# Kernel optimization log

Measured on AMD Instinct MI355X. Metric: run time of the kernel, lower is better.

## Reference

```python
import jax, jax.numpy as jnp
import numpy as np

B, C, H, W = 8, 96, 56, 56
N = H * W
K = 9
EPS = 1e-5

def _inorm(x):
    # InstanceNorm2d(affine=False): normalize over spatial dims per (batch, channel)
    m = jnp.mean(x, axis=(2, 3), keepdims=True)
    v = jnp.var(x, axis=(2, 3), keepdims=True)
    return (x - m) * jax.lax.rsqrt(v + EPS)

def _conv1(x, w, b):
    # 1x1 conv: (B,Cin,H,W) x (Cout,Cin) -> (B,Cout,H,W)
    return jnp.einsum('bchw,oc->bohw', x, w) + b[None, :, None, None]

def _grapher(x, rp, fc1_w, fc1_b, mr_w, mr_b, fc2_w, fc2_b):
    shortcut = x
    x = _inorm(_conv1(x, fc1_w, fc1_b))
    b, c, h, w = x.shape
    n = h * w
    xf = x.reshape(b, c, n)  # (B,C,N)
    # dynamic kNN on l2-normalized, gradient-stopped features (torch.no_grad + detach)
    xn = jax.lax.stop_gradient(xf)
    xn = xn / jnp.maximum(jnp.linalg.norm(xn, axis=1, keepdims=True), 1e-12)
    xt = jnp.swapaxes(xn, 1, 2)  # (B,N,C)
    sq = jnp.sum(xt * xt, axis=-1, keepdims=True)  # (B,N,1)
    dist = sq - 2.0 * jnp.einsum('bnc,bmc->bnm', xt, xt) + jnp.swapaxes(sq, 1, 2)
    dist = dist + rp  # relative_pos bias added to distances
    _, nn_idx = jax.lax.top_k(-dist, K)  # (B,N,K)
    # max-relative graph conv: gather neighbors, max over (x_j - x_i)
    x_j = jnp.take_along_axis(xf[:, :, None, :], nn_idx[:, None, :, :], axis=3)  # (B,C,N,K)
    xm = jnp.max(x_j - xf[:, :, :, None], axis=-1)  # (B,C,N)
    # channel-interleaved concat: (B,C,2,N,1) -> (B,2C,N,1)
    y = jnp.stack([xf, xm], axis=2).reshape(b, 2 * c, n, 1)
    y = jax.nn.gelu(_inorm(_conv1(y, mr_w, mr_b)), approximate=False)
    y = y.reshape(b, 2 * c, h, w)
    y = _inorm(_conv1(y, fc2_w, fc2_b))
    return y + shortcut

def _ffn(x, w1, b1, w2, b2):
    shortcut = x
    x = jax.nn.gelu(_inorm(_conv1(x, w1, b1)), approximate=False)
    x = _inorm(_conv1(x, w2, b2))
    return x + shortcut

_PARAM_SHAPES = [
    ('g1_fc1_w', (C, C)), ('g1_fc1_b', (C,)), ('g1_mr_w', (2*C, 2*C)), ('g1_mr_b', (2*C,)),
    ('g1_fc2_w', (C, 2*C)), ('g1_fc2_b', (C,)),
    ('g2_fc1_w', (C, C)), ('g2_fc1_b', (C,)), ('g2_mr_w', (2*C, 2*C)), ('g2_mr_b', (2*C,)),
    ('g2_fc2_w', (C, 2*C)), ('g2_fc2_b', (C,)),
    ('f1_fc1_w', (4*C, C)), ('f1_fc1_b', (4*C,)), ('f1_fc2_w', (C, 4*C)), ('f1_fc2_b', (C,)),
    ('f2_fc1_w', (4*C, C)), ('f2_fc1_b', (4*C,)), ('f2_fc2_w', (C, 4*C)), ('f2_fc2_b', (C,)),
]

def setup_inputs():
    key = jax.random.key(0)
    ks = jax.random.split(key, 2 + len(_PARAM_SHAPES))
    inp = {
        'x': jax.random.normal(ks[0], (B, C, H, W), dtype=jnp.float32),
        'relative_pos': jax.random.normal(ks[1], (1, N, N), dtype=jnp.float32) * 0.1,
    }
    for i, (nm, shp) in enumerate(_PARAM_SHAPES):
        inp[nm] = jax.random.normal(ks[i + 2], shp, dtype=jnp.float32) * 0.02
    return inp

def reference(x, relative_pos,
              g1_fc1_w, g1_fc1_b, g1_mr_w, g1_mr_b, g1_fc2_w, g1_fc2_b,
              g2_fc1_w, g2_fc1_b, g2_mr_w, g2_mr_b, g2_fc2_w, g2_fc2_b,
              f1_fc1_w, f1_fc1_b, f1_fc2_w, f1_fc2_b,
              f2_fc1_w, f2_fc1_b, f2_fc2_w, f2_fc2_b):
    y = _grapher(x, relative_pos, g1_fc1_w, g1_fc1_b, g1_mr_w, g1_mr_b, g1_fc2_w, g1_fc2_b)
    y = _ffn(y, f1_fc1_w, f1_fc1_b, f1_fc2_w, f1_fc2_b)
    y = jax.nn.relu(_inorm(y))
    y = _grapher(y, relative_pos, g2_fc1_w, g2_fc1_b, g2_mr_w, g2_mr_b, g2_fc2_w, g2_fc2_b)
    y = _ffn(y, f2_fc1_w, f2_fc1_b, f2_fc2_w, f2_fc2_b)
    y = _inorm(y)
    return x + y
```

## Files before the change

kernel.cpp:

```cpp
#include <hip/hip_runtime.h>
#include <math.h>

#define NN 3136
#define CC 96
#define BB 8
#define KNB 9
#define PARTS 7
#define FLT_MAX_ 3.402823466e+38f
typedef unsigned long long u64;

__global__ __launch_bounds__(256) void conv1_kernel(
    const float* __restrict__ in, const float* __restrict__ w,
    const float* __restrict__ bias, float* __restrict__ out, int K, int O)
{
    __shared__ float sW[16][64];
    __shared__ float sX[16][64];
    const int b  = blockIdx.z;
    const int n0 = blockIdx.x * 64;
    const int o0 = blockIdx.y * 64;
    const int tid = threadIdx.x;
    const int tx = tid & 15, ty = tid >> 4;
    const float* inb = in + (size_t)b * K * NN;

    float acc[4][4] = {{0.f}};

    for (int kb = 0; kb < K; kb += 16) {
        __syncthreads();
        {
            int o  = tid >> 2;
            int k4 = (tid & 3) << 2;
            float4 wv = make_float4(0.f, 0.f, 0.f, 0.f);
            if (o0 + o < O)
                wv = *(const float4*)&w[(size_t)(o0 + o) * K + kb + k4];
            sW[k4 + 0][o] = wv.x; sW[k4 + 1][o] = wv.y;
            sW[k4 + 2][o] = wv.z; sW[k4 + 3][o] = wv.w;
        }
        #pragma unroll
        for (int i = 0; i < 4; i++) {
            int e = tid + i * 256;
            int kk = e >> 6, n2 = e & 63;
            sX[kk][n2] = inb[(size_t)(kb + kk) * NN + n0 + n2];
        }
        __syncthreads();
        #pragma unroll
        for (int kk = 0; kk < 16; kk++) {
            const float4 av = *(const float4*)&sW[kk][ty << 2];
            const float4 xv = *(const float4*)&sX[kk][tx << 2];
            float a_[4] = {av.x, av.y, av.z, av.w};
            float x_[4] = {xv.x, xv.y, xv.z, xv.w};
            #pragma unroll
            for (int i = 0; i < 4; i++)
                #pragma unroll
                for (int j = 0; j < 4; j++)
                    acc[i][j] = fmaf(a_[i], x_[j], acc[i][j]);
        }
    }
    #pragma unroll
    for (int i = 0; i < 4; i++) {
        int o = o0 + (ty << 2) + i;
        if (o < O) {
            float bo = bias[o];
            float4 v = make_float4(acc[i][0] + bo, acc[i][1] + bo,
                                   acc[i][2] + bo, acc[i][3] + bo);
            *(float4*)&out[((size_t)b * O + o) * NN + n0 + (tx << 2)] = v;
        }
    }
}

__global__ __launch_bounds__(256) void inorm_kernel(
    const float* __restrict__ in, float* __restrict__ out,
    const float* __restrict__ res, int act)
{
    const int row = blockIdx.x;
    const float* x = in + (size_t)row * NN;
    const int tid = threadIdx.x;

    float v[13];
    float s = 0.f;
    #pragma unroll
    for (int i = 0; i < 13; i++) {
        int idx = tid + i * 256;
        v[i] = (idx < NN) ? x[idx] : 0.f;
        s += v[i];
    }
    __shared__ float red[4];
    #pragma unroll
    for (int off = 32; off > 0; off >>= 1) s += __shfl_down(s, off);
    if ((tid & 63) == 0) red[tid >> 6] = s;
    __syncthreads();
    const float mean = (red[0] + red[1] + red[2] + red[3]) * (1.f / (float)NN);

    float s2 = 0.f;
    #pragma unroll
    for (int i = 0; i < 13; i++) {
        int idx = tid + i * 256;
        if (idx < NN) { float d = v[i] - mean; s2 = fmaf(d, d, s2); }
    }
    #pragma unroll
    for (int off = 32; off > 0; off >>= 1) s2 += __shfl_down(s2, off);
    __syncthreads();
    if ((tid & 63) == 0) red[tid >> 6] = s2;
    __syncthreads();
    const float var = (red[0] + red[1] + red[2] + red[3]) * (1.f / (float)NN);
    const float rs = rsqrtf(var + 1e-5f);

    float* o = out + (size_t)row * NN;
    const float* rr = res ? (res + (size_t)row * NN) : nullptr;
    #pragma unroll
    for (int i = 0; i < 13; i++) {
        int idx = tid + i * 256;
        if (idx < NN) {
            float y = (v[i] - mean) * rs;
            if (act == 1)      y = 0.5f * y * (1.f + erff(y * 0.70710678118654752f));
            else if (act == 2) y = fmaxf(y, 0.f);
            if (rr) y += rr[idx];
            o[idx] = y;
        }
    }
}

__global__ __launch_bounds__(256) void colnorm_kernel(
    const float* __restrict__ xf, float* __restrict__ xn,
    float* __restrict__ sqc)
{
    const int g = blockIdx.x * 256 + threadIdx.x;
    const int b = g / NN;
    const int n = g - b * NN;
    const float* p = xf + (size_t)b * CC * NN + n;
    float* q = xn + (size_t)b * CC * NN + n;

    float s = 0.f;
    for (int c = 0; c < CC; c++) { float t = p[(size_t)c * NN]; s = fmaf(t, t, s); }
    const float den = fmaxf(sqrtf(s), 1e-12f);

    float sq = 0.f;
    for (int c = 0; c < CC; c++) {
        float t = p[(size_t)c * NN] / den;
        q[(size_t)c * NN] = t;
        sq = fmaf(t, t, sq);
    }
    sqc[g] = sq;
}

__device__ __forceinline__ u64 dkey(float d, int m)
{
    unsigned int ub = __float_as_uint(d);
    ub ^= (unsigned int)(((int)ub) >> 31) | 0x80000000u;
    return ((u64)ub << 32) | (unsigned int)m;
}
__device__ __forceinline__ void ins9u(u64 (&kk)[9], u64 key)
{
    if (key < kk[8]) {
        kk[8] = key;
        #pragma unroll
        for (int j = 8; j > 0; --j) {
            if (kk[j] < kk[j - 1]) {
                u64 t = kk[j]; kk[j] = kk[j - 1]; kk[j - 1] = t;
            }
        }
    }
}

__global__ __launch_bounds__(256) void knn_fused_kernel(
    const float* __restrict__ xn, const float* __restrict__ sqc,
    const float* __restrict__ rp, u64* __restrict__ pko)
{
    __shared__ float shR[CC * 64];
    __shared__ float shC[CC * 64];
    const int b    = blockIdx.z;
    const int part = blockIdx.y;
    const int r0   = blockIdx.x * 64;
    const int tid  = threadIdx.x;
    const int tx = tid & 7;
    const int ty = tid >> 3;
    const float* xb  = xn  + (size_t)b * CC * NN;
    const float* sqb = sqc + (size_t)b * NN;

    #pragma unroll
    for (int i = 0; i < 6; i++) {
        int idx = tid + i * 256;
        int c = idx >> 4, r4 = (idx & 15) << 2;
        *(float4*)&shR[c * 64 + r4] = *(const float4*)&xb[(size_t)c * NN + r0 + r4];
    }

    u64 kk0[9], kk1[9];
    #pragma unroll
    for (int j = 0; j < 9; j++) { kk0[j] = kk1[j] = 0xFFFFFFFFFFFFFFFFull; }

    const int rA = r0 + ty * 2;

    for (int mt = 0; mt < PARTS; mt++) {
        const int m0 = (part * PARTS + mt) * 64;

        const float4 s0 = *(const float4*)&sqb[m0 + tx * 8];
        const float4 s1 = *(const float4*)&sqb[m0 + tx * 8 + 4];
        const float4 a0 = *(const float4*)&rp[(size_t)rA * NN + m0 + tx * 8];
        const float4 a1 = *(const float4*)&rp[(size_t)rA * NN + m0 + tx * 8 + 4];
        const float4 b0v = *(const float4*)&rp[(size_t)(rA + 1) * NN + m0 + tx * 8];
        const float4 b1v = *(const float4*)&rp[(size_t)(rA + 1) * NN + m0 + tx * 8 + 4];

        __syncthreads();
        #pragma unroll
        for (int i = 0; i < 6; i++) {
            int idx = tid + i * 256;
            int c = idx >> 4, m4 = (idx & 15) << 2;
            *(float4*)&shC[c * 64 + m4] =
                *(const float4*)&xb[(size_t)c * NN + m0 + m4];
        }
        __syncthreads();

        float acc0[8] = {0.f, 0.f, 0.f, 0.f, 0.f, 0.f, 0.f, 0.f};
        float acc1[8] = {0.f, 0.f, 0.f, 0.f, 0.f, 0.f, 0.f, 0.f};
        #pragma unroll 4
        for (int c = 0; c < CC; c++) {
            const float2 rv = *(const float2*)&shR[c * 64 + ty * 2];
            const float4 c0 = *(const float4*)&shC[c * 64 + tx * 8];
            const float4 c1 = *(const float4*)&shC[c * 64 + tx * 8 + 4];
            acc0[0] = fmaf(rv.x, c0.x, acc0[0]);
            acc0[1] = fmaf(rv.x, c0.y, acc0[1]);
            acc0[2] = fmaf(rv.x, c0.z, acc0[2]);
            acc0[3] = fmaf(rv.x, c0.w, acc0[3]);
            acc0[4] = fmaf(rv.x, c1.x, acc0[4]);
            acc0[5] = fmaf(rv.x, c1.y, acc0[5]);
            acc0[6] = fmaf(rv.x, c1.z, acc0[6]);
            acc0[7] = fmaf(rv.x, c1.w, acc0[7]);
            acc1[0] = fmaf(rv.y, c0.x, acc1[0]);
            acc1[1] = fmaf(rv.y, c0.y, acc1[1]);
            acc1[2] = fmaf(rv.y, c0.z, acc1[2]);
            acc1[3] = fmaf(rv.y, c0.w, acc1[3]);
            acc1[4] = fmaf(rv.y, c1.x, acc1[4]);
            acc1[5] = fmaf(rv.y, c1.y, acc1[5]);
            acc1[6] = fmaf(rv.y, c1.z, acc1[6]);
            acc1[7] = fmaf(rv.y, c1.w, acc1[7]);
        }

        const float sq_[8] = {s0.x, s0.y, s0.z, s0.w, s1.x, s1.y, s1.z, s1.w};
        const float rA_[8] = {a0.x, a0.y, a0.z, a0.w, a1.x, a1.y, a1.z, a1.w};
        const float rB_[8] = {b0v.x, b0v.y, b0v.z, b0v.w, b1v.x, b1v.y, b1v.z, b1v.w};
        #pragma unroll
        for (int j = 0; j < 8; j++) {
            const int m = m0 + tx * 8 + j;
            ins9u(kk0, dkey(fmaf(-2.f, acc0[j], sq_[j] + rA_[j]), m));
            ins9u(kk1, dkey(fmaf(-2.f, acc1[j], sq_[j] + rB_[j]), m));
        }
    }

    const size_t base0 = ((size_t)(b * NN + rA)     * PARTS + part) * KNB;
    const size_t base1 = ((size_t)(b * NN + rA + 1) * PARTS + part) * KNB;
    #pragma unroll
    for (int k = 0; k < 9; k++) {
        u64 w = kk0[0];
        #pragma unroll
        for (int off = 1; off < 8; off <<= 1) {
            unsigned int lo = __shfl_xor((unsigned int)w, off);
            unsigned int hi = __shfl_xor((unsigned int)(w >> 32), off);
            u64 o = ((u64)hi << 32) | lo;
            w = (o < w) ? o : w;
        }
        if (kk0[0] == w) {
            #pragma unroll
            for (int j = 0; j < 8; j++) kk0[j] = kk0[j + 1];
            kk0[8] = 0xFFFFFFFFFFFFFFFFull;
        }
        if (tx == 0) pko[base0 + k] = w;
    }
    #pragma unroll
    for (int k = 0; k < 9; k++) {
        u64 w = kk1[0];
        #pragma unroll
        for (int off = 1; off < 8; off <<= 1) {
            unsigned int lo = __shfl_xor((unsigned int)w, off);
            unsigned int hi = __shfl_xor((unsigned int)(w >> 32), off);
            u64 o = ((u64)hi << 32) | lo;
            w = (o < w) ? o : w;
        }
        if (kk1[0] == w) {
            #pragma unroll
            for (int j = 0; j < 8; j++) kk1[j] = kk1[j + 1];
            kk1[8] = 0xFFFFFFFFFFFFFFFFull;
        }
        if (tx == 0) pko[base1 + k] = w;
    }
}

__global__ __launch_bounds__(256) void knn_merge_kernel(
    const u64* __restrict__ pko, int* __restrict__ nn_idx)
{
    const int g = blockIdx.x * 256 + threadIdx.x;
    if (g >= BB * NN) return;
    u64 kk[9];
    #pragma unroll
    for (int j = 0; j < 9; j++) kk[j] = 0xFFFFFFFFFFFFFFFFull;
    const u64* v = pko + (size_t)g * PARTS * KNB;
    for (int p = 0; p < PARTS; p++)
        #pragma unroll
        for (int j = 0; j < 9; j++)
            ins9u(kk, v[p * KNB + j]);
    #pragma unroll
    for (int j = 0; j < 9; j++)
        nn_idx[(size_t)g * KNB + j] = (int)(kk[j] & 0xFFFFFFFFu);
}

__global__ __launch_bounds__(256) void gather_kernel(
    const float* __restrict__ xf, const int* __restrict__ nn_idx,
    float* __restrict__ y)
{
    const size_t g = (size_t)blockIdx.x * 256 + threadIdx.x;
    const int n  = (int)(g % NN);
    const int bc = (int)(g / NN);
    const int c  = bc % CC;
    const int b  = bc / CC;
    const float* row = xf + (size_t)(b * CC + c) * NN;
    const float xi = row[n];
    const int* id = nn_idx + ((size_t)b * NN + n) * KNB;
    float mx = -FLT_MAX_;
    #pragma unroll
    for (int k = 0; k < KNB; k++) mx = fmaxf(mx, row[id[k]] - xi);
    float* o = y + ((size_t)b * 2 * CC + 2 * c) * NN + n;
    o[0]  = xi;
    o[NN] = mx;
}

static void conv1(const float* in, const float* w, const float* b, float* out,
                  int K, int O, hipStream_t s)
{
    dim3 grid(NN / 64, (O + 63) / 64, BB);
    conv1_kernel<<<grid, 256, 0, s>>>(in, w, b, out, K, O);
}
static void inorm(const float* in, float* out, const float* res, int ch, int act,
                  hipStream_t s)
{
    inorm_kernel<<<BB * ch, 256, 0, s>>>(in, out, res, act);
}

struct GrapherP {
    const float *fc1w, *fc1b, *mrw, *mrb, *fc2w, *fc2b;
};

static void run_grapher(const float* in, const float* rp, const GrapherP& p,
                        float* outCur, float* bufA, float* bufB, float* xnb,
                        float* sqc, int* idx, hipStream_t s)
{
    conv1(in, p.fc1w, p.fc1b, bufA, CC, CC, s);
    inorm(bufA, bufB, nullptr, CC, 0, s);
    colnorm_kernel<<<(BB * NN) / 256, 256, 0, s>>>(bufB, xnb, sqc);
    u64* pko = (u64*)bufA;
    knn_fused_kernel<<<dim3(NN / 64, PARTS, BB), 256, 0, s>>>(xnb, sqc, rp, pko);
    knn_merge_kernel<<<(BB * NN + 255) / 256, 256, 0, s>>>(pko, idx);
    gather_kernel<<<(BB * CC * NN) / 256, 256, 0, s>>>(bufB, idx, bufA);
    conv1(bufA, p.mrw, p.mrb, bufB, 2 * CC, 2 * CC, s);
    inorm(bufB, bufA, nullptr, 2 * CC, 1, s);
    conv1(bufA, p.fc2w, p.fc2b, bufB, 2 * CC, CC, s);
    inorm(bufB, outCur, in, CC, 0, s);
}

static void run_ffn(const float* in, const float* w1, const float* b1,
                    const float* w2, const float* b2,
                    float* outCur, float* bufA, float* bufB, hipStream_t s)
{
    conv1(in, w1, b1, bufA, CC, 4 * CC, s);
    inorm(bufA, bufB, nullptr, 4 * CC, 1, s);
    conv1(bufB, w2, b2, bufA, 2 * CC * 2, CC, s);
    inorm(bufA, outCur, in, CC, 0, s);
}

extern "C" void kernel_launch(void* const* d_in, const int* in_sizes, int n_in,
                              void* d_out, int out_size, void* d_ws, size_t ws_size,
                              hipStream_t stream)
{
    const float* x  = (const float*)d_in[0];
    const float* rp = (const float*)d_in[1];
    GrapherP g1 = {(const float*)d_in[2],  (const float*)d_in[3],
                   (const float*)d_in[4],  (const float*)d_in[5],
                   (const float*)d_in[6],  (const float*)d_in[7]};
    GrapherP g2 = {(const float*)d_in[8],  (const float*)d_in[9],
                   (const float*)d_in[10], (const float*)d_in[11],
                   (const float*)d_in[12], (const float*)d_in[13]};
    const float* f1w1 = (const float*)d_in[14]; const float* f1b1 = (const float*)d_in[15];
    const float* f1w2 = (const float*)d_in[16]; const float* f1b2 = (const float*)d_in[17];
    const float* f2w1 = (const float*)d_in[18]; const float* f2b1 = (const float*)d_in[19];
    const float* f2w2 = (const float*)d_in[20]; const float* f2b2 = (const float*)d_in[21];
    float* out = (float*)d_out;

    const size_t P  = (size_t)BB * CC * NN;
    const size_t P4 = 4 * P;
    float* ws   = (float*)d_ws;
    float* bufA = ws;
    float* bufB = bufA + P4;
    float* xnb  = bufB + P4;
    float* cur0 = xnb + P;
    float* cur1 = cur0 + P;
    float* sqc  = cur1 + P;
    int*   idx  = (int*)(sqc + (size_t)BB * NN);

    run_grapher(x, rp, g1, cur0, bufA, bufB, xnb, sqc, idx, stream);
    run_ffn(cur0, f1w1, f1b1, f1w2, f1b2, cur1, bufA, bufB, stream);
    inorm(cur1, cur0, nullptr, CC, 2, stream);
    run_grapher(cur0, rp, g2, cur1, bufA, bufB, xnb, sqc, idx, stream);
    run_ffn(cur1, f2w1, f2b1, f2w2, f2b2, cur0, bufA, bufB, stream);
    inorm(cur0, out, x, CC, 0, stream);
    (void)in_sizes; (void)n_in; (void)out_size; (void)ws_size;
}
```

Baseline: 1.300 ms.

## Retile kNN distance kernel to 4x4 per thread and prefetch next column tile

Changes the kNN distance tile so each thread computes 4 rows by 4 columns instead of 2 by 8. Each thread now keeps four 9-entry top-k lists, and the final shuffle reduction runs across 16 lanes instead of 8. The next column tile of features is also prefetched into registers while the current tile is computed, to hide global load latency. This raises register pressure substantially (36 u64 top-k entries per thread), which may lower occupancy or cause spills, and it doubles the number of insertion lists each thread maintains.

```diff
diff --git a/kernel.cpp b/kernel.cpp
--- a/kernel.cpp
+++ b/kernel.cpp
@@ -171,8 +171,8 @@
     const int part = blockIdx.y;
     const int r0   = blockIdx.x * 64;
     const int tid  = threadIdx.x;
-    const int tx = tid & 7;
-    const int ty = tid >> 3;
+    const int tx = tid & 15;
+    const int ty = tid >> 4;
     const float* xb  = xn  + (size_t)b * CC * NN;
     const float* sqb = sqc + (size_t)b * NN;
 
@@ -183,103 +183,99 @@
         *(float4*)&shR[c * 64 + r4] = *(const float4*)&xb[(size_t)c * NN + r0 + r4];
     }
 
-    u64 kk0[9], kk1[9];
-    #pragma unroll
-    for (int j = 0; j < 9; j++) { kk0[j] = kk1[j] = 0xFFFFFFFFFFFFFFFFull; }
-
-    const int rA = r0 + ty * 2;
-
-    for (int mt = 0; mt < PARTS; mt++) {
-        const int m0 = (part * PARTS + mt) * 64;
-
-        const float4 s0 = *(const float4*)&sqb[m0 + tx * 8];
-        const float4 s1 = *(const float4*)&sqb[m0 + tx * 8 + 4];
-        const float4 a0 = *(const float4*)&rp[(size_t)rA * NN + m0 + tx * 8];
-        const float4 a1 = *(const float4*)&rp[(size_t)rA * NN + m0 + tx * 8 + 4];
-        const float4 b0v = *(const float4*)&rp[(size_t)(rA + 1) * NN + m0 + tx * 8];
-        const float4 b1v = *(const float4*)&rp[(size_t)(rA + 1) * NN + m0 + tx * 8 + 4];
-
-        __syncthreads();
+    u64 kk[4][9];
+    #pragma unroll
+    for (int i = 0; i < 4; i++)
+        #pragma unroll
+        for (int j = 0; j < 9; j++) kk[i][j] = 0xFFFFFFFFFFFFFFFFull;
+
+    const int rA = r0 + ty * 4;
+
+    float4 nx[6];
+    {
+        const int m0 = part * PARTS * 64;
         #pragma unroll
         for (int i = 0; i < 6; i++) {
             int idx = tid + i * 256;
             int c = idx >> 4, m4 = (idx & 15) << 2;
-            *(float4*)&shC[c * 64 + m4] =
-                *(const float4*)&xb[(size_t)c * NN + m0 + m4];
-        }
+            nx[i] = *(const float4*)&xb[(size_t)c * NN + m0 + m4];
+        }
+    }
+
+    for (int mt = 0; mt < PARTS; mt++) {
+        const int m0 = (part * PARTS + mt) * 64;
+
         __syncthreads();
-
-        float acc0[8] = {0.f, 0.f, 0.f, 0.f, 0.f, 0.f, 0.f, 0.f};
-        float acc1[8] = {0.f, 0.f, 0.f, 0.f, 0.f, 0.f, 0.f, 0.f};
+        #pragma unroll
+        for (int i = 0; i < 6; i++) {
+            int idx = tid + i * 256;
+            int c = idx >> 4, m4 = (idx & 15) << 2;
+            *(float4*)&shC[c * 64 + m4] = nx[i];
+        }
+        if (mt + 1 < PARTS) {
+            const int m0n = m0 + 64;
+            #pragma unroll
+            for (int i = 0; i < 6; i++) {
+                int idx = tid + i * 256;
+                int c = idx >> 4, m4 = (idx & 15) << 2;
+                nx[i] = *(const float4*)&xb[(size_t)c * NN + m0n + m4];
+            }
+        }
+        const float4 sqv = *(const float4*)&sqb[m0 + tx * 4];
+        const float4 rp0 = *(const float4*)&rp[(size_t)(rA + 0) * NN + m0 + tx * 4];
+        const float4 rp1 = *(const float4*)&rp[(size_t)(rA + 1) * NN + m0 + tx * 4];
+        const float4 rp2 = *(const float4*)&rp[(size_t)(rA + 2) * NN + m0 + tx * 4];
+        const float4 rp3 = *(const float4*)&rp[(size_t)(rA + 3) * NN + m0 + tx * 4];
+        __syncthreads();
+
+        float acc[4][4] = {{0.f}};
         #pragma unroll 4
         for (int c = 0; c < CC; c++) {
-            const float2 rv = *(const float2*)&shR[c * 64 + ty * 2];
-            const float4 c0 = *(const float4*)&shC[c * 64 + tx * 8];
-            const float4 c1 = *(const float4*)&shC[c * 64 + tx * 8 + 4];
-            acc0[0] = fmaf(rv.x, c0.x, acc0[0]);
-            acc0[1] = fmaf(rv.x, c0.y, acc0[1]);
-            acc0[2] = fmaf(rv.x, c0.z, acc0[2]);
-            acc0[3] = fmaf(rv.x, c0.w, acc0[3]);
-            acc0[4] = fmaf(rv.x, c1.x, acc0[4]);
-            acc0[5] = fmaf(rv.x, c1.y, acc0[5]);
-            acc0[6] = fmaf(rv.x, c1.z, acc0[6]);
-            acc0[7] = fmaf(rv.x, c1.w, acc0[7]);
-            acc1[0] = fmaf(rv.y, c0.x, acc1[0]);
-            acc1[1] = fmaf(rv.y, c0.y, acc1[1]);
-            acc1[2] = fmaf(rv.y, c0.z, acc1[2]);
-            acc1[3] = fmaf(rv.y, c0.w, acc1[3]);
-            acc1[4] = fmaf(rv.y, c1.x, acc1[4]);
-            acc1[5] = fmaf(rv.y, c1.y, acc1[5]);
-            acc1[6] = fmaf(rv.y, c1.z, acc1[6]);
-            acc1[7] = fmaf(rv.y, c1.w, acc1[7]);
-        }
-
-        const float sq_[8] = {s0.x, s0.y, s0.z, s0.w, s1.x, s1.y, s1.z, s1.w};
-        const float rA_[8] = {a0.x, a0.y, a0.z, a0.w, a1.x, a1.y, a1.z, a1.w};
-        const float rB_[8] = {b0v.x, b0v.y, b0v.z, b0v.w, b1v.x, b1v.y, b1v.z, b1v.w};
-        #pragma unroll
-        for (int j = 0; j < 8; j++) {
-            const int m = m0 + tx * 8 + j;
-            ins9u(kk0, dkey(fmaf(-2.f, acc0[j], sq_[j] + rA_[j]), m));
-            ins9u(kk1, dkey(fmaf(-2.f, acc1[j], sq_[j] + rB_[j]), m));
-        }
-    }
-
-    const size_t base0 = ((size_t)(b * NN + rA)     * PARTS + part) * KNB;
-    const size_t base1 = ((size_t)(b * NN + rA + 1) * PARTS + part) * KNB;
-    #pragma unroll
-    for (int k = 0; k < 9; k++) {
-        u64 w = kk0[0];
-        #pragma unroll
-        for (int off = 1; off < 8; off <<= 1) {
-            unsigned int lo = __shfl_xor((unsigned int)w, off);
-            unsigned int hi = __shfl_xor((unsigned int)(w >> 32), off);
-            u64 o = ((u64)hi << 32) | lo;
-            w = (o < w) ? o : w;
-        }
-        if (kk0[0] == w) {
-            #pragma unroll
-            for (int j = 0; j < 8; j++) kk0[j] = kk0[j + 1];
-            kk0[8] = 0xFFFFFFFFFFFFFFFFull;
-        }
-        if (tx == 0) pko[base0 + k] = w;
-    }
-    #pragma unroll
-    for (int k = 0; k < 9; k++) {
-        u64 w = kk1[0];
-        #pragma unroll
-        for (int off = 1; off < 8; off <<= 1) {
-            unsigned int lo = __shfl_xor((unsigned int)w, off);
-            unsigned int hi = __shfl_xor((unsigned int)(w >> 32), off);
-            u64 o = ((u64)hi << 32) | lo;
-            w = (o < w) ? o : w;
-        }
-        if (kk1[0] == w) {
-            #pragma unroll
-            for (int j = 0; j < 8; j++) kk1[j] = kk1[j + 1];
-            kk1[8] = 0xFFFFFFFFFFFFFFFFull;
-        }
-        if (tx == 0) pko[base1 + k] = w;
+            const float4 rv = *(const float4*)&shR[c * 64 + ty * 4];
+            const float4 cv = *(const float4*)&shC[c * 64 + tx * 4];
+            const float r_[4] = {rv.x, rv.y, rv.z, rv.w};
+            const float c_[4] = {cv.x, cv.y, cv.z, cv.w};
+            #pragma unroll
+            for (int i = 0; i < 4; i++)
+                #pragma unroll
+                for (int j = 0; j < 4; j++)
+                    acc[i][j] = fmaf(r_[i], c_[j], acc[i][j]);
+        }
+
+        const float sq_[4] = {sqv.x, sqv.y, sqv.z, sqv.w};
+        const float rpv[4][4] = {{rp0.x, rp0.y, rp0.z, rp0.w},
+                                 {rp1.x, rp1.y, rp1.z, rp1.w},
+                                 {rp2.x, rp2.y, rp2.z, rp2.w},
+                                 {rp3.x, rp3.y, rp3.z, rp3.w}};
+        #pragma unroll
+        for (int i = 0; i < 4; i++)
+            #pragma unroll
+            for (int j = 0; j < 4; j++) {
+                const int m = m0 + tx * 4 + j;
+                ins9u(kk[i], dkey(fmaf(-2.f, acc[i][j], sq_[j] + rpv[i][j]), m));
+            }
+    }
+
+    #pragma unroll
+    for (int i = 0; i < 4; i++) {
+        const size_t base = ((size_t)(b * NN + rA + i) * PARTS + part) * KNB;
+        #pragma unroll
+        for (int k = 0; k < 9; k++) {
+            u64 w = kk[i][0];
+            #pragma unroll
+            for (int off = 1; off < 16; off <<= 1) {
+                unsigned int lo = __shfl_xor((unsigned int)w, off);
+                unsigned int hi = __shfl_xor((unsigned int)(w >> 32), off);
+                u64 o = ((u64)hi << 32) | lo;
+                w = (o < w) ? o : w;
+            }
+            if (kk[i][0] == w) {
+                #pragma unroll
+                for (int j = 0; j < 8; j++) kk[i][j] = kk[i][j + 1];
+                kk[i][8] = 0xFFFFFFFFFFFFFFFFull;
+            }
+            if (tx == 0) pko[base + k] = w;
+        }
     }
 }
 
```

Measured after the change: 1.509 ms. 1.16x slower.

## Compute kNN distance Gram matrix with bf16x3 split MFMA instead of FP32 FMA

Applied to the files above, without the earlier changes.

Normalized features are split into three bf16 parts (high, mid, low) and stored row-major. The kNN kernel then computes the pairwise dot products with six 16x16x32 bf16 MFMA products per K chunk, which approximates FP32 accuracy, replacing the scalar FP32 FMA tile loop. The block grows to 512 threads, each handling one row and 4 columns per 32-column tile, with results staged through shared memory before top-9 insertion. The aim is to move the dominant N^2*C GEMM onto matrix cores. The cost is extra split/conversion work, more syncs per tile, and a small risk of precision-induced neighbor tie flips.

```diff
diff --git a/kernel.cpp b/kernel.cpp
--- a/kernel.cpp
+++ b/kernel.cpp
@@ -8,6 +8,9 @@
 #define PARTS 7
 #define FLT_MAX_ 3.402823466e+38f
 typedef unsigned long long u64;
+typedef unsigned short ushortT;
+typedef __attribute__((ext_vector_type(8))) short short8;
+typedef __attribute__((ext_vector_type(4))) float f32x4;
 
 __global__ __launch_bounds__(256) void conv1_kernel(
     const float* __restrict__ in, const float* __restrict__ w,
@@ -119,25 +122,41 @@
     }
 }
 
+__device__ __forceinline__ unsigned bf16rne(float x)
+{
+    unsigned u = __float_as_uint(x);
+    return (u + 0x7fffu + ((u >> 16) & 1u)) >> 16;
+}
+
 __global__ __launch_bounds__(256) void colnorm_kernel(
-    const float* __restrict__ xf, float* __restrict__ xn,
+    const float* __restrict__ xf, ushortT* __restrict__ xh,
+    ushortT* __restrict__ xm, ushortT* __restrict__ xl,
     float* __restrict__ sqc)
 {
     const int g = blockIdx.x * 256 + threadIdx.x;
     const int b = g / NN;
     const int n = g - b * NN;
     const float* p = xf + (size_t)b * CC * NN + n;
-    float* q = xn + (size_t)b * CC * NN + n;
 
     float s = 0.f;
     for (int c = 0; c < CC; c++) { float t = p[(size_t)c * NN]; s = fmaf(t, t, s); }
     const float den = fmaxf(sqrtf(s), 1e-12f);
 
+    const size_t o = (size_t)g * CC;
     float sq = 0.f;
     for (int c = 0; c < CC; c++) {
         float t = p[(size_t)c * NN] / den;
-        q[(size_t)c * NN] = t;
         sq = fmaf(t, t, sq);
+        unsigned hr = bf16rne(t);
+        float hf = __uint_as_float(hr << 16);
+        float r1 = t - hf;
+        unsigned mr = bf16rne(r1);
+        float mf = __uint_as_float(mr << 16);
+        float r2 = r1 - mf;
+        unsigned lr = bf16rne(r2);
+        xh[o + c] = (ushortT)hr;
+        xm[o + c] = (ushortT)mr;
+        xl[o + c] = (ushortT)lr;
     }
     sqc[g] = sq;
 }
@@ -161,125 +180,112 @@
     }
 }
 
-__global__ __launch_bounds__(256) void knn_fused_kernel(
-    const float* __restrict__ xn, const float* __restrict__ sqc,
+__global__ __launch_bounds__(512, 4) void knn_mfma_kernel(
+    const ushortT* __restrict__ xh, const ushortT* __restrict__ xm,
+    const ushortT* __restrict__ xl, const float* __restrict__ sqc,
     const float* __restrict__ rp, u64* __restrict__ pko)
 {
-    __shared__ float shR[CC * 64];
-    __shared__ float shC[CC * 64];
+    __shared__ ushortT shA[3][64][104];
+    __shared__ ushortT shB[3][32][104];
+    __shared__ float   shD[64][33];
     const int b    = blockIdx.z;
     const int part = blockIdx.y;
     const int r0   = blockIdx.x * 64;
     const int tid  = threadIdx.x;
+    const int ty = tid >> 3;
     const int tx = tid & 7;
-    const int ty = tid >> 3;
-    const float* xb  = xn  + (size_t)b * CC * NN;
+    const int w  = tid >> 6;
+    const int l  = tid & 63;
+    const int Rt = w & 3;
+    const int Mt = w >> 2;
+    const int fr = l & 15;
+    const int fq = l >> 4;
     const float* sqb = sqc + (size_t)b * NN;
 
     #pragma unroll
-    for (int i = 0; i < 6; i++) {
-        int idx = tid + i * 256;
-        int c = idx >> 4, r4 = (idx & 15) << 2;
-        *(float4*)&shR[c * 64 + r4] = *(const float4*)&xb[(size_t)c * NN + r0 + r4];
-    }
-
-    u64 kk0[9], kk1[9];
-    #pragma unroll
-    for (int j = 0; j < 9; j++) { kk0[j] = kk1[j] = 0xFFFFFFFFFFFFFFFFull; }
-
-    const int rA = r0 + ty * 2;
-
-    for (int mt = 0; mt < PARTS; mt++) {
-        const int m0 = (part * PARTS + mt) * 64;
-
-        const float4 s0 = *(const float4*)&sqb[m0 + tx * 8];
-        const float4 s1 = *(const float4*)&sqb[m0 + tx * 8 + 4];
-        const float4 a0 = *(const float4*)&rp[(size_t)rA * NN + m0 + tx * 8];
-        const float4 a1 = *(const float4*)&rp[(size_t)rA * NN + m0 + tx * 8 + 4];
-        const float4 b0v = *(const float4*)&rp[(size_t)(rA + 1) * NN + m0 + tx * 8];
-        const float4 b1v = *(const float4*)&rp[(size_t)(rA + 1) * NN + m0 + tx * 8 + 4];
-
+    for (int i = 0; i < 5; i++) {
+        int idx = tid + i * 512;
+        if (idx < 2304) {
+            int s = idx / 768, rem = idx - s * 768;
+            int r = rem / 12, cc = (rem - r * 12) * 8;
+            const ushortT* bp = (s == 0) ? xh : ((s == 1) ? xm : xl);
+            *(float4*)&shA[s][r][cc] =
+                *(const float4*)&bp[((size_t)(b * NN + r0 + r)) * CC + cc];
+        }
+    }
+
+    u64 kk0[9];
+    #pragma unroll
+    for (int j = 0; j < 9; j++) kk0[j] = 0xFFFFFFFFFFFFFFFFull;
+
+    for (int mt = 0; mt < 14; mt++) {
+        const int m0 = part * 448 + mt * 32;
+
+        #pragma unroll
+        for (int i = 0; i < 3; i++) {
+            int idx = tid + i * 512;
+            if (idx < 1152) {
+                int s = idx / 384, rem = idx - s * 384;
+                int m = rem / 12, cc = (rem - m * 12) * 8;
+                const ushortT* bp = (s == 0) ? xh : ((s == 1) ? xm : xl);
+                *(float4*)&shB[s][m][cc] =
+                    *(const float4*)&bp[((size_t)(b * NN + m0 + m)) * CC + cc];
+            }
+        }
+        const float4 sqv = *(const float4*)&sqb[m0 + tx * 4];
+        const float4 rpv = *(const float4*)&rp[(size_t)(r0 + ty) * NN + m0 + tx * 4];
         __syncthreads();
-        #pragma unroll
-        for (int i = 0; i < 6; i++) {
-            int idx = tid + i * 256;
-            int c = idx >> 4, m4 = (idx & 15) << 2;
-            *(float4*)&shC[c * 64 + m4] =
-                *(const float4*)&xb[(size_t)c * NN + m0 + m4];
-        }
+
+        f32x4 acc = {0.f, 0.f, 0.f, 0.f};
+        #pragma unroll
+        for (int kc = 0; kc < 3; kc++) {
+            const int ca = kc * 32 + fq * 8;
+            const short8 ah = *(const short8*)&shA[0][Rt * 16 + fr][ca];
+            const short8 am = *(const short8*)&shA[1][Rt * 16 + fr][ca];
+            const short8 al = *(const short8*)&shA[2][Rt * 16 + fr][ca];
+            const short8 bh = *(const short8*)&shB[0][Mt * 16 + fr][ca];
+            const short8 bm = *(const short8*)&shB[1][Mt * 16 + fr][ca];
+            const short8 bl = *(const short8*)&shB[2][Mt * 16 + fr][ca];
+            acc = __builtin_amdgcn_mfma_f32_16x16x32_bf16(ah, bh, acc, 0, 0, 0);
+            acc = __builtin_amdgcn_mfma_f32_16x16x32_bf16(ah, bm, acc, 0, 0, 0);
+            acc = __builtin_amdgcn_mfma_f32_16x16x32_bf16(am, bh, acc, 0, 0, 0);
+            acc = __builtin_amdgcn_mfma_f32_16x16x32_bf16(am, bm, acc, 0, 0, 0);
+            acc = __builtin_amdgcn_mfma_f32_16x16x32_bf16(ah, bl, acc, 0, 0, 0);
+            acc = __builtin_amdgcn_mfma_f32_16x16x32_bf16(al, bh, acc, 0, 0, 0);
+        }
+        #pragma unroll
+        for (int q = 0; q < 4; q++)
+            shD[Rt * 16 + fq * 4 + q][Mt * 16 + fr] = acc[q];
         __syncthreads();
 
-        float acc0[8] = {0.f, 0.f, 0.f, 0.f, 0.f, 0.f, 0.f, 0.f};
-        float acc1[8] = {0.f, 0.f, 0.f, 0.f, 0.f, 0.f, 0.f, 0.f};
-        #pragma unroll 4
-        for (int c = 0; c < CC; c++) {
-            const float2 rv = *(const float2*)&shR[c * 64 + ty * 2];
-            const float4 c0 = *(const float4*)&shC[c * 64 + tx * 8];
-            const float4 c1 = *(const float4*)&shC[c * 64 + tx * 8 + 4];
-            acc0[0] = fmaf(rv.x, c0.x, acc0[0]);
-            acc0[1] = fmaf(rv.x, c0.y, acc0[1]);
-            acc0[2] = fmaf(rv.x, c0.z, acc0[2]);
-            acc0[3] = fmaf(rv.x, c0.w, acc0[3]);
-            acc0[4] = fmaf(rv.x, c1.x, acc0[4]);
-            acc0[5] = fmaf(rv.x, c1.y, acc0[5]);
-            acc0[6] = fmaf(rv.x, c1.z, acc0[6]);
-            acc0[7] = fmaf(rv.x, c1.w, acc0[7]);
-            acc1[0] = fmaf(rv.y, c0.x, acc1[0]);
-            acc1[1] = fmaf(rv.y, c0.y, acc1[1]);
-            acc1[2] = fmaf(rv.y, c0.z, acc1[2]);
-            acc1[3] = fmaf(rv.y, c0.w, acc1[3]);
-            acc1[4] = fmaf(rv.y, c1.x, acc1[4]);
-            acc1[5] = fmaf(rv.y, c1.y, acc1[5]);
-            acc1[6] = fmaf(rv.y, c1.z, acc1[6]);
-            acc1[7] = fmaf(rv.y, c1.w, acc1[7]);
-        }
-
-        const float sq_[8] = {s0.x, s0.y, s0.z, s0.w, s1.x, s1.y, s1.z, s1.w};
-        const float rA_[8] = {a0.x, a0.y, a0.z, a0.w, a1.x, a1.y, a1.z, a1.w};
-        const float rB_[8] = {b0v.x, b0v.y, b0v.z, b0v.w, b1v.x, b1v.y, b1v.z, b1v.w};
-        #pragma unroll
-        for (int j = 0; j < 8; j++) {
-            const int m = m0 + tx * 8 + j;
-            ins9u(kk0, dkey(fmaf(-2.f, acc0[j], sq_[j] + rA_[j]), m));
-            ins9u(kk1, dkey(fmaf(-2.f, acc1[j], sq_[j] + rB_[j]), m));
-        }
-    }
-
-    const size_t base0 = ((size_t)(b * NN + rA)     * PARTS + part) * KNB;
-    const size_t base1 = ((size_t)(b * NN + rA + 1) * PARTS + part) * KNB;
+        const float d0 = shD[ty][tx * 4 + 0];
+        const float d1 = shD[ty][tx * 4 + 1];
+        const float d2 = shD[ty][tx * 4 + 2];
+        const float d3 = shD[ty][tx * 4 + 3];
+        const int mb = m0 + tx * 4;
+        ins9u(kk0, dkey(fmaf(-2.f, d0, sqv.x + rpv.x), mb + 0));
+        ins9u(kk0, dkey(fmaf(-2.f, d1, sqv.y + rpv.y), mb + 1));
+        ins9u(kk0, dkey(fmaf(-2.f, d2, sqv.z + rpv.z), mb + 2));
+        ins9u(kk0, dkey(fmaf(-2.f, d3, sqv.w + rpv.w), mb + 3));
+    }
+
+    const size_t base = ((size_t)(b * NN + r0 + ty) * PARTS + part) * KNB;
     #pragma unroll
     for (int k = 0; k < 9; k++) {
-        u64 w = kk0[0];
+        u64 wv = kk0[0];
         #pragma unroll
         for (int off = 1; off < 8; off <<= 1) {
-            unsigned int lo = __shfl_xor((unsigned int)w, off);
-            unsigned int hi = __shfl_xor((unsigned int)(w >> 32), off);
+            unsigned int lo = __shfl_xor((unsigned int)wv, off);
+            unsigned int hi = __shfl_xor((unsigned int)(wv >> 32), off);
             u64 o = ((u64)hi << 32) | lo;
-            w = (o < w) ? o : w;
-        }
-        if (kk0[0] == w) {
+            wv = (o < wv) ? o : wv;
+        }
+        if (kk0[0] == wv) {
             #pragma unroll
             for (int j = 0; j < 8; j++) kk0[j] = kk0[j + 1];
             kk0[8] = 0xFFFFFFFFFFFFFFFFull;
         }
-        if (tx == 0) pko[base0 + k] = w;
-    }
-    #pragma unroll
-    for (int k = 0; k < 9; k++) {
-        u64 w = kk1[0];
-        #pragma unroll
-        for (int off = 1; off < 8; off <<= 1) {
-            unsigned int lo = __shfl_xor((unsigned int)w, off);
-            unsigned int hi = __shfl_xor((unsigned int)(w >> 32), off);
-            u64 o = ((u64)hi << 32) | lo;
-            w = (o < w) ? o : w;
-        }
-        if (kk1[0] == w) {
-            #pragma unroll
-            for (int j = 0; j < 8; j++) kk1[j] = kk1[j + 1];
-            kk1[8] = 0xFFFFFFFFFFFFFFFFull;
-        }
-        if (tx == 0) pko[base1 + k] = w;
+        if (tx == 0) pko[base + k] = wv;
     }
 }
 
@@ -338,14 +344,16 @@
 };
 
 static void run_grapher(const float* in, const float* rp, const GrapherP& p,
-                        float* outCur, float* bufA, float* bufB, float* xnb,
+                        float* outCur, float* bufA, float* bufB,
+                        ushortT* xh, ushortT* xm, ushortT* xl,
                         float* sqc, int* idx, hipStream_t s)
 {
     conv1(in, p.fc1w, p.fc1b, bufA, CC, CC, s);
     inorm(bufA, bufB, nullptr, CC, 0, s);
-    colnorm_kernel<<<(BB * NN) / 256, 256, 0, s>>>(bufB, xnb, sqc);
+    colnorm_kernel<<<(BB * NN) / 256, 256, 0, s>>>(bufB, xh, xm, xl, sqc);
     u64* pko = (u64*)bufA;
-    knn_fused_kernel<<<dim3(NN / 64, PARTS, BB), 256, 0, s>>>(xnb, sqc, rp, pko);
+    knn_mfma_kernel<<<dim3(NN / 64, PARTS, BB), 512, 0, s>>>(
+        xh, xm, xl, sqc, rp, pko);
     knn_merge_kernel<<<(BB * NN + 255) / 256, 256, 0, s>>>(pko, idx);
     gather_kernel<<<(BB * CC * NN) / 256, 256, 0, s>>>(bufB, idx, bufA);
     conv1(bufA, p.mrw, p.mrb, bufB, 2 * CC, 2 * CC, s);
@@ -387,16 +395,18 @@
     float* ws   = (float*)d_ws;
     float* bufA = ws;
     float* bufB = bufA + P4;
-    float* xnb  = bufB + P4;
-    float* cur0 = xnb + P;
+    float* cur0 = bufB + P4;
     float* cur1 = cur0 + P;
     float* sqc  = cur1 + P;
     int*   idx  = (int*)(sqc + (size_t)BB * NN);
-
-    run_grapher(x, rp, g1, cur0, bufA, bufB, xnb, sqc, idx, stream);
+    ushortT* xh = (ushortT*)(idx + (size_t)BB * NN * KNB);
+    ushortT* xm = xh + P;
+    ushortT* xl = xm + P;
+
+    run_grapher(x, rp, g1, cur0, bufA, bufB, xh, xm, xl, sqc, idx, stream);
     run_ffn(cur0, f1w1, f1b1, f1w2, f1b2, cur1, bufA, bufB, stream);
     inorm(cur1, cur0, nullptr, CC, 2, stream);
-    run_grapher(cur0, rp, g2, cur1, bufA, bufB, xnb, sqc, idx, stream);
+    run_grapher(cur0, rp, g2, cur1, bufA, bufB, xh, xm, xl, sqc, idx, stream);
     run_ffn(cur1, f2w1, f2b1, f2w2, f2b2, cur0, bufA, bufB, stream);
     inorm(cur0, out, x, CC, 0, stream);
     (void)in_sizes; (void)n_in; (void)out_size; (void)ws_size;
```

After: 1.160 ms. -10.8%, faster.
